# Performance work log

Hardware: AMD Instinct MI355X
Metric: run time of the kernel (lower is better)

## Reference

```python
import jax, jax.numpy as jnp
import numpy as np

B, S, H, M = 8, 4096, 1024, 1024
TEMP = 1.0


def setup_inputs() -> dict:
    key = jax.random.key(0)
    ks = jax.random.split(key, 6)
    sd = 1.0 / np.sqrt(H)
    return {
        "hidden_states": jax.random.normal(ks[0], (B, S, H), jnp.float32),
        "Wq": jax.random.normal(ks[1], (H, H), jnp.float32) * sd,
        "bq": jnp.zeros((H,), jnp.float32),
        "Wk": jax.random.normal(ks[2], (H, H), jnp.float32) * sd,
        "bk": jnp.zeros((H,), jnp.float32),
        "Wv": jax.random.normal(ks[3], (H, H), jnp.float32) * sd,
        "bv": jnp.zeros((H,), jnp.float32),
        "Wo": jax.random.normal(ks[4], (H, 2 * H), jnp.float32) * (1.0 / np.sqrt(2 * H)),
        "bo": jnp.zeros((H,), jnp.float32),
    }


def _l2_normalize(x, eps=1e-12):
    # matches F.normalize(p=2, dim=-1): x / max(||x||, eps)
    n = jnp.sqrt(jnp.sum(x * x, axis=-1, keepdims=True))
    return x / jnp.maximum(n, eps)


def reference(hidden_states, Wq, bq, Wk, bk, Wv, bv, Wo, bo):
    b, s, h = hidden_states.shape
    # _initialize_memory: evenly sample M positions along seq (seq_len >= memory_size)
    idx = jnp.linspace(0.0, s - 1, M).astype(jnp.int32)
    init_states = hidden_states[:, idx]                 # [B, M, H]
    memory_keys = init_states @ Wk.T + bk               # [B, M, H]
    memory_values = init_states @ Wv.T + bv             # [B, M, H]

    query_keys = hidden_states @ Wq.T + bq              # [B, S, H]
    qn = _l2_normalize(query_keys)
    kn = _l2_normalize(memory_keys)
    sim = jnp.einsum('bsh,bmh->bsm', qn, kn) / TEMP     # cosine similarity
    attn = jax.nn.softmax(sim, axis=-1)                 # [B, S, M]
    retrieved = jnp.einsum('bsm,bmh->bsh', attn, memory_values)

    combined = jnp.concatenate([hidden_states, retrieved], axis=-1)  # [B, S, 2H]
    enhanced = combined @ Wo.T + bo                     # [B, S, H]
    return enhanced
```

## Files before the change

kernel.cpp:

```cpp
#include <hip/hip_runtime.h>
#include <hip/hip_bf16.h>
#include <type_traits>
#include <stdint.h>

#define AS1 __attribute__((address_space(1)))
#define AS3 __attribute__((address_space(3)))

typedef __attribute__((ext_vector_type(8))) short short8;
typedef __attribute__((ext_vector_type(4))) short short4v;
typedef __attribute__((ext_vector_type(4))) float floatx4;

#define B_DIM 8
#define S_DIM 4096
#define H_DIM 1024
#define M_DIM 1024

__device__ __forceinline__ float b2f(short s) {
  union { unsigned u; float f; } x;
  x.u = ((unsigned)(unsigned short)s) << 16;
  return x.f;
}
__device__ __forceinline__ short f2b(float f) {
  union { float f; unsigned u; } x;
  x.f = f;
  unsigned u = x.u;
  unsigned r = (u + 0x7fffu + ((u >> 16) & 1u)) >> 16;
  return (short)(unsigned short)r;
}

#define SCHEDB() __builtin_amdgcn_sched_barrier(0)
#define VMCNT(N) asm volatile("s_waitcnt vmcnt(" #N ")")
#define BARRIER() do { SCHEDB(); __builtin_amdgcn_s_barrier(); SCHEDB(); } while (0)

__device__ __forceinline__ void async16(const void* g, void* l) {
  __builtin_amdgcn_global_load_lds((const AS1 void*)g, (AS3 void*)l, 16, 0, 0);
}

__global__ __launch_bounds__(256) void k_cvt(const float4* __restrict__ in,
                                             short4v* __restrict__ out, int n4) {
  const int stride = gridDim.x * 256;
  for (int i = blockIdx.x * 256 + threadIdx.x; i < n4; i += stride) {
    float4 v = in[i];
    short4v o = { f2b(v.x), f2b(v.y), f2b(v.z), f2b(v.w) };
    out[i] = o;
  }
}

__global__ __launch_bounds__(256) void k_cvtw(const float4* __restrict__ Wq,
                                              const float4* __restrict__ Wk,
                                              const float4* __restrict__ Wv,
                                              const float4* __restrict__ Wo,
                                              short4v* __restrict__ wq,
                                              short4v* __restrict__ wk,
                                              short4v* __restrict__ wv,
                                              short4v* __restrict__ wo) {
  const int stride = gridDim.x * 256;
  for (int i = blockIdx.x * 256 + threadIdx.x; i < 1310720; i += stride) {
    const float4* src; short4v* dst; int j;
    if (i < 262144)      { src = Wq; dst = wq; j = i; }
    else if (i < 524288) { src = Wk; dst = wk; j = i - 262144; }
    else if (i < 786432) { src = Wv; dst = wv; j = i - 524288; }
    else                 { src = Wo; dst = wo; j = i - 786432; }
    float4 v = src[j];
    short4v o = { f2b(v.x), f2b(v.y), f2b(v.z), f2b(v.w) };
    dst[j] = o;
  }
}

template<int AMODE, int EPI, bool HAS_BIAS, typename OutT>
__global__ __launch_bounds__(512, 2)
void k_gemm256(const short* __restrict__ A, const short* __restrict__ A2,
               const short* __restrict__ Bw,
               const float* __restrict__ bias, const float* __restrict__ bias2,
               OutT* __restrict__ C, short* __restrict__ Cv,
               int K, long sA, long sB, long sC)
{
  __shared__ __align__(16) short lds[2][2][256 * 64];

  const int t512 = threadIdx.x;
  const int l = t512 & 63;
  const int w = t512 >> 6;
  const int wm = w >> 2, wn = w & 3;
  const int z = blockIdx.z;

  const int gx = gridDim.x, gy = gridDim.y;
  const int orig = blockIdx.y * gx + blockIdx.x;
  const int nwg = gx * gy;
  int s = orig;
  if ((nwg & 7) == 0) {
    const int q8 = nwg >> 3;
    s = (orig & 7) * q8 + (orig >> 3);
  }
  const int row0 = (s / gy) * 256;
  const int col0 = (s % gy) * 256;

  const short* Az = A + (size_t)z * sA;
  const short* Bz = Bw + (size_t)z * sB;

  const int rloc = t512 >> 3;
  const int slot = t512 & 7;
  const int sw = slot ^ (rloc & 7);
  const int nt = K >> 6;

  const int lr = l & 15;
  const int lkb = (l >> 4) << 4;
  const int aswz = (lr & 7) << 4;
  const int aRowByte = (wm * 128 + lr) * 128;
  const int bRowByte = (wn * 64 + lr) * 128;

  auto srcA = [&](int R, int tile) -> const char* {
    if constexpr (AMODE == 2) {
      const size_t row = (size_t)(row0 + R + rloc);
      if (tile < 16) return (const char*)A  + ((row * 1024 + (size_t)tile * 64) << 1) + (sw << 4);
      else           return (const char*)A2 + ((row * 1024 + (size_t)(tile - 16) * 64) << 1) + (sw << 4);
    } else if constexpr (AMODE == 1) {
      const int r = row0 + R + rloc;
      const unsigned m = (unsigned)(r & (M_DIM - 1));
      const int g = (r >> 10) * S_DIM + (int)((m * 4095u) / 1023u);
      return (const char*)A + (((size_t)g * H_DIM + (size_t)tile * 64) << 1) + (sw << 4);
    } else {
      return (const char*)Az + (((size_t)(row0 + R + rloc) * K + (size_t)tile * 64) << 1) + (sw << 4);
    }
  };
  auto srcB = [&](int R, int tile) -> const char* {
    return (const char*)Bz + (((size_t)(col0 + R + rloc) * K + (size_t)tile * 64) << 1) + (sw << 4);
  };
  auto SA = [&](int buf, int R, int tile) {
    async16(srcA(R, tile), (char*)&lds[buf][0][0] + (size_t)(R + w * 8) * 128);
  };
  auto SB = [&](int buf, int R, int tile) {
    async16(srcB(R, tile), (char*)&lds[buf][1][0] + (size_t)(R + w * 8) * 128);
  };

  floatx4 acc[8][4];
  #pragma unroll
  for (int i = 0; i < 8; ++i)
    #pragma unroll
    for (int j = 0; j < 4; ++j)
      acc[i][j] = (floatx4){0.f, 0.f, 0.f, 0.f};

  {
    const int t1 = (nt > 1) ? 1 : 0;
    SA(0, 0, 0);  SA(0, 64, 0); SA(0, 128, 0); SA(0, 192, 0);
    SB(0, 0, 0);  SB(0, 64, 0); SB(0, 128, 0); SB(0, 192, 0);
    SA(1, 0, t1); SA(1, 128, t1);
    SB(1, 0, t1); SB(1, 64, t1); SB(1, 128, t1); SB(1, 192, t1);
    SCHEDB();
    VMCNT(6);
    BARRIER();
  }

#define RD_A(Mh, ks)                                                              \
  {                                                                               \
    _Pragma("unroll")                                                             \
    for (int mi = 0; mi < 4; ++mi)                                                \
      af[mi] = *(const short8*)(ldsAb + aRowByte + (Mh) * 8192 + mi * 2048 +      \
                                ((((ks) * 64) + lkb) ^ aswz));                    \
  }
#define RD_B(ks)                                                                  \
  {                                                                               \
    _Pragma("unroll")                                                             \
    for (int ni = 0; ni < 4; ++ni)                                                \
      bf[ni] = *(const short8*)(ldsBb + bRowByte + ni * 2048 +                    \
                                ((((ks) * 64) + lkb) ^ aswz));                    \
  }
#define PH_MFMA(Mh)                                                               \
  {                                                                               \
    __builtin_amdgcn_s_setprio(1);                                                \
    _Pragma("unroll")                                                             \
    for (int mi = 0; mi < 4; ++mi)                                                \
      _Pragma("unroll")                                                           \
      for (int ni = 0; ni < 4; ++ni)                                              \
        acc[(Mh) * 4 + mi][ni] = __builtin_amdgcn_mfma_f32_16x16x32_bf16(         \
            af[mi], bf[ni], acc[(Mh) * 4 + mi][ni], 0, 0, 0);                     \
    __builtin_amdgcn_s_setprio(0);                                                \
  }

  for (int t = 0; t < nt; ++t) {
    const int b = t & 1;
    const char* ldsAb = (const char*)&lds[b][0][0];
    const char* ldsBb = (const char*)&lds[b][1][0];
    const int tn  = (t + 1 < nt) ? t + 1 : nt - 1;
    const int tn2 = (t + 2 < nt) ? t + 2 : nt - 1;
    short8 af[4], bf[4];

    RD_A(0, 0); RD_B(0);
    SA(b ^ 1, 64, tn); SA(b ^ 1, 192, tn);
    BARRIER();
    PH_MFMA(0);
    SCHEDB();
    VMCNT(8);
    BARRIER();

    RD_A(1, 0);
    BARRIER();
    PH_MFMA(1);
    BARRIER();

    RD_A(0, 1); RD_B(1);
    BARRIER();
    PH_MFMA(0);
    BARRIER();

    RD_A(1, 1);
    SA(b, 0, tn2); SA(b, 128, tn2);
    SB(b, 0, tn2); SB(b, 64, tn2); SB(b, 128, tn2); SB(b, 192, tn2);
    BARRIER();
    PH_MFMA(1);
    SCHEDB();
    VMCNT(8);
    BARRIER();
  }
#undef RD_A
#undef RD_B
#undef PH_MFMA

  SCHEDB();
  VMCNT(0);
  SCHEDB();

  OutT* Cz = C + (size_t)z * sC;
  const int rsub = (l >> 4) * 4;
  #pragma unroll
  for (int ni = 0; ni < 4; ++ni) {
    const int colg = col0 + wn * 64 + ni * 16 + lr;
    float bvv = 0.f;
    if constexpr (HAS_BIAS) {
      if constexpr (EPI == 1) bvv = (colg < 1024) ? bias[colg] : bias2[colg - 1024];
      else bvv = bias[colg];
    }
    #pragma unroll
    for (int m = 0; m < 8; ++m) {
      const int rg = row0 + wm * 128 + (m >> 2) * 64 + (m & 3) * 16 + rsub;
      #pragma unroll
      for (int j = 0; j < 4; ++j) {
        const float v = acc[m][ni][j] + bvv;
        const int rr = rg + j;
        if constexpr (EPI == 1) {
          if (colg < 1024) {
            ((short*)C)[(size_t)rr * 1024 + colg] = f2b(v);
          } else {
            const int bb = rr >> 10, mm = rr & (M_DIM - 1);
            Cv[((size_t)bb * H_DIM + (colg - 1024)) * M_DIM + mm] = f2b(v);
          }
        } else {
          const size_t o = (size_t)rr * 1024 + colg;
          if constexpr (std::is_same<OutT, float>::value) Cz[o] = v;
          else Cz[o] = f2b(v);
        }
      }
    }
  }
}

__global__ __launch_bounds__(256) void k_rownorm(const short* __restrict__ x,
                                                 float* __restrict__ inv) {
  const int w = threadIdx.x >> 6, l = threadIdx.x & 63;
  const size_t row = (size_t)blockIdx.x * 4 + w;
  const short* p = x + row * 1024 + l * 16;
  short8 v0 = *(const short8*)p;
  short8 v1 = *(const short8*)(p + 8);
  float ss = 0.f;
  #pragma unroll
  for (int i = 0; i < 8; ++i) {
    const float a = b2f(v0[i]), b = b2f(v1[i]);
    ss += a * a + b * b;
  }
  #pragma unroll
  for (int o = 32; o > 0; o >>= 1) ss += __shfl_xor(ss, o, 64);
  if (l == 0) inv[row] = 1.f / fmaxf(sqrtf(ss), 1e-12f);
}

__global__ __launch_bounds__(256) void k_softmax(short* __restrict__ sbuf,
                                                 const float* __restrict__ qinv,
                                                 const float* __restrict__ kinv) {
  const int w = threadIdx.x >> 6, l = threadIdx.x & 63;
  const size_t row = (size_t)blockIdx.x * 4 + w;
  short* p = sbuf + row * 1024 + l * 16;
  const float qi = qinv[row];
  const float* kv = kinv + ((row >> 12) << 10) + l * 16;
  float ki[16];
  *(float4*)&ki[0]  = *(const float4*)(kv);
  *(float4*)&ki[4]  = *(const float4*)(kv + 4);
  *(float4*)&ki[8]  = *(const float4*)(kv + 8);
  *(float4*)&ki[12] = *(const float4*)(kv + 12);
  short8 v0 = *(short8*)p;
  short8 v1 = *(short8*)(p + 8);
  float f[16];
  #pragma unroll
  for (int i = 0; i < 8; ++i) {
    f[i]     = b2f(v0[i]) * qi * ki[i];
    f[8 + i] = b2f(v1[i]) * qi * ki[8 + i];
  }
  float mx = f[0];
  #pragma unroll
  for (int i = 1; i < 16; ++i) mx = fmaxf(mx, f[i]);
  #pragma unroll
  for (int o = 32; o > 0; o >>= 1) mx = fmaxf(mx, __shfl_xor(mx, o, 64));
  float s = 0.f;
  #pragma unroll
  for (int i = 0; i < 16; ++i) { f[i] = __expf(f[i] - mx); s += f[i]; }
  #pragma unroll
  for (int o = 32; o > 0; o >>= 1) s += __shfl_xor(s, o, 64);
  const float inv = 1.f / s;
  #pragma unroll
  for (int i = 0; i < 8; ++i) { v0[i] = f2b(f[i] * inv); v1[i] = f2b(f[8 + i] * inv); }
  *(short8*)p = v0;
  *(short8*)(p + 8) = v1;
}

extern "C" void kernel_launch(void* const* d_in, const int* in_sizes, int n_in,
                              void* d_out, int out_size, void* d_ws, size_t ws_size,
                              hipStream_t stream)
{
  const float* hid = (const float*)d_in[0];
  const float* Wq  = (const float*)d_in[1];
  const float* bq  = (const float*)d_in[2];
  const float* Wk  = (const float*)d_in[3];
  const float* bk  = (const float*)d_in[4];
  const float* Wv  = (const float*)d_in[5];
  const float* bv  = (const float*)d_in[6];
  const float* Wo  = (const float*)d_in[7];
  const float* bo  = (const float*)d_in[8];

  char* ws = (char*)d_ws;
  short* hb  = (short*)(ws);
  short* qb  = (short*)(ws + (size_t)67108864);
  short* knb = (short*)(ws + (size_t)134217728);
  short* mvT = (short*)(ws + (size_t)150994944);
  short* wqb = (short*)(ws + (size_t)167772160);
  short* wkb = (short*)(ws + (size_t)169869312);
  short* wvb = (short*)(ws + (size_t)171966464);
  short* wob = (short*)(ws + (size_t)174063616);
  short* sb  = (short*)d_out;
  float* qinv = (float*)((char*)d_out + (size_t)67108864);
  float* kinv = (float*)((char*)d_out + (size_t)67108864 + 131072);
  short* rb  = qb;
  float* out = (float*)d_out;

  k_cvt<<<4096, 256, 0, stream>>>((const float4*)hid, (short4v*)hb, 33554432 / 4);
  k_cvtw<<<1280, 256, 0, stream>>>((const float4*)Wq, (const float4*)Wk,
                                   (const float4*)Wv, (const float4*)Wo,
                                   (short4v*)wqb, (short4v*)wkb, (short4v*)wvb, (short4v*)wob);

  k_gemm256<0, 0, true, short><<<dim3(128, 4, 1), 512, 0, stream>>>(
      hb, nullptr, wqb, bq, nullptr, qb, nullptr, 1024, 0, 0, 0);
  k_gemm256<1, 1, true, short><<<dim3(32, 8, 1), 512, 0, stream>>>(
      hb, nullptr, wkb, bk, bv, knb, mvT, 1024, 0, 0, 0);
  k_rownorm<<<8192, 256, 0, stream>>>(qb, qinv);
  k_rownorm<<<2048, 256, 0, stream>>>(knb, kinv);
  k_gemm256<0, 0, false, short><<<dim3(16, 4, 8), 512, 0, stream>>>(
      qb, nullptr, knb, nullptr, nullptr, sb, nullptr, 1024,
      (long)S_DIM * H_DIM, (long)M_DIM * H_DIM, (long)S_DIM * M_DIM);
  k_softmax<<<8192, 256, 0, stream>>>(sb, qinv, kinv);
  k_gemm256<0, 0, false, short><<<dim3(16, 4, 8), 512, 0, stream>>>(
      sb, nullptr, mvT, nullptr, nullptr, rb, nullptr, 1024,
      (long)S_DIM * M_DIM, (long)H_DIM * M_DIM, (long)S_DIM * H_DIM);
  k_gemm256<2, 0, true, float><<<dim3(128, 4, 1), 512, 0, stream>>>(
      hb, rb, wob, bo, nullptr, out, nullptr, 2048, 0, 0, 0);
}
```

Measured before the change: 528.4 us.

## Double-buffer MFMA fragment registers to overlap LDS reads with matrix math

Restructures the GEMM main loop so LDS fragment reads for the next phase are issued before the current phase's MFMAs, using two A and two B fragment register sets (afX/afY, bf0/bf1). The first fragments of the next tile are prefetched from the other LDS buffer at the end of each iteration, and the vmcnt waits are retuned to match. The aim is to hide LDS read latency behind MFMA execution. It costs extra VGPRs, which could lower occupancy, and the retuned wait counts and barriers need to be exactly right to avoid races.

```diff
diff --git a/kernel.cpp b/kernel.cpp
--- a/kernel.cpp
+++ b/kernel.cpp
@@ -150,21 +150,21 @@
     BARRIER();
   }
 
-#define RD_A(Mh, ks)                                                              \
+#define RD_A4(dst, ldsbase, Mh, ks)                                               \
   {                                                                               \
     _Pragma("unroll")                                                             \
     for (int mi = 0; mi < 4; ++mi)                                                \
-      af[mi] = *(const short8*)(ldsAb + aRowByte + (Mh) * 8192 + mi * 2048 +      \
-                                ((((ks) * 64) + lkb) ^ aswz));                    \
-  }
-#define RD_B(ks)                                                                  \
+      dst[mi] = *(const short8*)((ldsbase) + aRowByte + (Mh) * 8192 +             \
+                                 mi * 2048 + ((((ks) * 64) + lkb) ^ aswz));       \
+  }
+#define RD_B4(dst, ldsbase, ks)                                                   \
   {                                                                               \
     _Pragma("unroll")                                                             \
     for (int ni = 0; ni < 4; ++ni)                                                \
-      bf[ni] = *(const short8*)(ldsBb + bRowByte + ni * 2048 +                    \
-                                ((((ks) * 64) + lkb) ^ aswz));                    \
-  }
-#define PH_MFMA(Mh)                                                               \
+      dst[ni] = *(const short8*)((ldsbase) + bRowByte + ni * 2048 +               \
+                                 ((((ks) * 64) + lkb) ^ aswz));                   \
+  }
+#define MFMA16(Mh, av, bv)                                                        \
   {                                                                               \
     __builtin_amdgcn_s_setprio(1);                                                \
     _Pragma("unroll")                                                             \
@@ -172,48 +172,60 @@
       _Pragma("unroll")                                                           \
       for (int ni = 0; ni < 4; ++ni)                                              \
         acc[(Mh) * 4 + mi][ni] = __builtin_amdgcn_mfma_f32_16x16x32_bf16(         \
-            af[mi], bf[ni], acc[(Mh) * 4 + mi][ni], 0, 0, 0);                     \
+            av[mi], bv[ni], acc[(Mh) * 4 + mi][ni], 0, 0, 0);                     \
     __builtin_amdgcn_s_setprio(0);                                                \
+  }
+
+  short8 afX[4], afY[4], bf0[4], bf1[4];
+
+  {
+    const char* L0A = (const char*)&lds[0][0][0];
+    const char* L0B = (const char*)&lds[0][1][0];
+    RD_A4(afX, L0A, 0, 0);
+    RD_B4(bf0, L0B, 0);
   }
 
   for (int t = 0; t < nt; ++t) {
     const int b = t & 1;
-    const char* ldsAb = (const char*)&lds[b][0][0];
-    const char* ldsBb = (const char*)&lds[b][1][0];
+    const char* LA  = (const char*)&lds[b][0][0];
+    const char* LB  = (const char*)&lds[b][1][0];
+    const char* LA1 = (const char*)&lds[b ^ 1][0][0];
+    const char* LB1 = (const char*)&lds[b ^ 1][1][0];
     const int tn  = (t + 1 < nt) ? t + 1 : nt - 1;
     const int tn2 = (t + 2 < nt) ? t + 2 : nt - 1;
-    short8 af[4], bf[4];
-
-    RD_A(0, 0); RD_B(0);
+
+    RD_A4(afY, LA, 1, 0);
     SA(b ^ 1, 64, tn); SA(b ^ 1, 192, tn);
     BARRIER();
-    PH_MFMA(0);
+    MFMA16(0, afX, bf0);
+    BARRIER();
+
+    RD_A4(afX, LA, 0, 1);
+    RD_B4(bf1, LB, 1);
+    BARRIER();
+    MFMA16(1, afY, bf0);
+    BARRIER();
+
+    RD_A4(afY, LA, 1, 1);
+    BARRIER();
+    MFMA16(0, afX, bf1);
     SCHEDB();
-    VMCNT(8);
-    BARRIER();
-
-    RD_A(1, 0);
-    BARRIER();
-    PH_MFMA(1);
-    BARRIER();
-
-    RD_A(0, 1); RD_B(1);
-    BARRIER();
-    PH_MFMA(0);
-    BARRIER();
-
-    RD_A(1, 1);
+    VMCNT(2);
+    BARRIER();
+
+    RD_A4(afX, LA1, 0, 0);
+    RD_B4(bf0, LB1, 0);
     SA(b, 0, tn2); SA(b, 128, tn2);
     SB(b, 0, tn2); SB(b, 64, tn2); SB(b, 128, tn2); SB(b, 192, tn2);
     BARRIER();
-    PH_MFMA(1);
+    MFMA16(1, afY, bf1);
     SCHEDB();
-    VMCNT(8);
-    BARRIER();
-  }
-#undef RD_A
-#undef RD_B
-#undef PH_MFMA
+    VMCNT(6);
+    BARRIER();
+  }
+#undef RD_A4
+#undef RD_B4
+#undef MFMA16
 
   SCHEDB();
   VMCNT(0);
```

Result: no change. 523.2 us (-1.0%).
